# Kernel optimization log

Measured on AMD Instinct MI355X. Metric: run time of the kernel, lower is better.

The kernel has to match this reference:

```python
import jax, jax.numpy as jnp
import numpy as np
import itertools

N_SET = 4        # number of elements in the input set (input.size(-2))
IN_F = 2048      # in_features
OUT_F = 2048     # out_features
BOT = 512        # bottleneck_dim
B = 512          # batch size
NUM_NODES = 391
EMB_DIM = 300

# All nonempty subsets of range(N_SET), ordered by scale then lexicographic,
# exactly matching the torch loop over scales / itertools.combinations.
SUBSETS = [c for s in range(1, N_SET + 1) for c in itertools.combinations(range(N_SET), s)]

def _incl_matrix():
    # M[i, j] = 1 if SUBSETS[j] is a subset of SUBSETS[i].
    # This reproduces the dict-based scatter-sum: the aggregated output for rset
    # is the sum of raw Relation outputs over all nonempty k \subseteq rset.
    masks = [sum(1 << i for i in c) for c in SUBSETS]
    n = len(masks)
    M = np.zeros((n, n), dtype=np.float32)
    for i, mi in enumerate(masks):
        for j, mj in enumerate(masks):
            if (mj & mi) == mj:
                M[i, j] = 1.0
    return M

INCL = _incl_matrix()  # [15, 15]

def setup_inputs():
    key = jax.random.key(0)
    ks = jax.random.split(key, 16)
    inp = {"x": jax.random.normal(ks[0], (B, N_SET, IN_F), dtype=jnp.float32)}
    ki = 1
    for s in range(1, N_SET + 1):
        fan = s * IN_F
        inp[f"w1_s{s}"] = jax.random.normal(ks[ki], (BOT, fan), dtype=jnp.float32) / np.float32(np.sqrt(fan)); ki += 1
        inp[f"b1_s{s}"] = jnp.zeros((BOT,), dtype=jnp.float32)
        inp[f"w2_s{s}"] = jax.random.normal(ks[ki], (OUT_F, BOT), dtype=jnp.float32) / np.float32(np.sqrt(BOT)); ki += 1
        inp[f"b2_s{s}"] = jnp.zeros((OUT_F,), dtype=jnp.float32)
    inp["w_emb"] = jax.random.normal(ks[ki], (EMB_DIM, OUT_F), dtype=jnp.float32) / np.float32(np.sqrt(OUT_F)); ki += 1
    inp["b_emb"] = jnp.zeros((EMB_DIM,), dtype=jnp.float32)
    inp["w_node"] = jax.random.normal(ks[ki], (NUM_NODES, OUT_F), dtype=jnp.float32) / np.float32(np.sqrt(OUT_F)); ki += 1
    inp["b_node"] = jnp.zeros((NUM_NODES,), dtype=jnp.float32)
    return inp

def _base_forward(x, ws):
    # Batched per-scale Relation MLPs over all C(4,s) subsets at once.
    raws = []
    for s in range(1, N_SET + 1):
        idx = np.array(list(itertools.combinations(range(N_SET), s)))  # [C, s]
        g = x[:, idx, :]                                  # [B, C, s, F] gather
        h = g.reshape(g.shape[0], g.shape[1], s * IN_F)   # concat along subset
        w1, b1, w2, b2 = ws[s - 1]
        h = jax.nn.relu(h)
        h = jax.nn.relu(jnp.einsum('bcf,of->bco', h, w1) + b1)
        raws.append(jnp.einsum('bcd,od->bco', h, w2) + b2)  # [B, C, OUT_F]
    raw = jnp.concatenate(raws, axis=1)  # [B, 15, OUT_F]
    # Subset-inclusion scatter-sum, expressed as a dense 15x15 contraction.
    return jnp.einsum('ij,bjf->bif', jnp.asarray(INCL), raw)

def reference(x, w1_s1, b1_s1, w2_s1, b2_s1, w1_s2, b1_s2, w2_s2, b2_s2,
              w1_s3, b1_s3, w2_s3, b2_s3, w1_s4, b1_s4, w2_s4, b2_s4,
              w_emb, b_emb, w_node, b_node):
    ws = [(w1_s1, b1_s1, w2_s1, b2_s1), (w1_s2, b1_s2, w2_s2, b2_s2),
          (w1_s3, b1_s3, w2_s3, b2_s3), (w1_s4, b1_s4, w2_s4, b2_s4)]
    feats = _base_forward(x, ws)                              # [B, 15, OUT_F]
    embeddings = jnp.einsum('bnf,ef->bne', feats, w_emb) + b_emb  # [B, 15, 300]
    node_out = jnp.einsum('bnf,vf->bnv', feats, w_node) + b_node  # [B, 15, 391]
    return embeddings, jnp.swapaxes(node_out, -2, -1)             # [B, 391, 15]
```

## Files before the change

kernel.cpp:

```cpp
#include <hip/hip_runtime.h>
#include <stdint.h>

using bf16x8 = __attribute__((ext_vector_type(8))) short;
using f32x4  = __attribute__((ext_vector_type(4))) float;

#define DEVINL __device__ __forceinline__

DEVINL unsigned short f2bf(float f) {
  union { float f; unsigned u; } v; v.f = f;
  unsigned u = v.u;
  return (unsigned short)((u + 0x7FFFu + ((u >> 16) & 1u)) >> 16);
}
DEVINL float bf2f(unsigned short h) {
  union { unsigned u; float f; } v; v.u = ((unsigned)h) << 16;
  return v.f;
}

DEVINL void gload_lds16(const void* g, void* l) {
  __builtin_amdgcn_global_load_lds(
      (const __attribute__((address_space(1))) void*)g,
      (__attribute__((address_space(3))) void*)l, 16, 0, 0);
}

template<int OUT_BF16, int HAS_BIAS>
DEVINL void gemm_core(const unsigned short* __restrict__ A,
                      const unsigned short* __restrict__ B,
                      void* __restrict__ C,
                      const float* __restrict__ bias,
                      int K, int Cld, int arow0, int brow0, int crow0, int ccol0)
{
  __shared__ __align__(16) unsigned short As[3][256 * 64];
  __shared__ __align__(16) unsigned short Bs[3][128 * 64];

  const int t    = threadIdx.x;
  const int wave = t >> 6;
  const int lane = t & 63;
  const int wr   = (wave >> 1) << 6;
  const int wc   = (wave & 1) << 6;
  const int lrow = lane & 15;
  const int kg   = lane >> 4;

  f32x4 acc[4][4];
#pragma unroll
  for (int r = 0; r < 4; ++r)
#pragma unroll
    for (int q = 0; q < 4; ++q) acc[r][q] = (f32x4){0.f, 0.f, 0.f, 0.f};

  const int srow = t >> 3;
  const int scol = (((t & 7) ^ (srow & 7)) << 3);
  const unsigned short* aSrc = A + (size_t)(arow0 + srow) * K + scol;
  const unsigned short* bSrc = B + (size_t)(brow0 + srow) * K + scol;

  auto STAGE_S0 = [&](int slot, int kt) {
    const int k0 = kt << 6;
    char* aD = (char*)As[slot] + wave * 1024;
    char* bD = (char*)Bs[slot] + wave * 1024;
    gload_lds16(aSrc + (size_t)0 * K + k0, aD);
    gload_lds16(aSrc + (size_t)64 * K + k0, aD + 8192);
    gload_lds16(bSrc + (size_t)0 * K + k0, bD);
  };
  auto STAGE_S1 = [&](int slot, int kt) {
    const int k0 = kt << 6;
    char* aD = (char*)As[slot] + wave * 1024;
    char* bD = (char*)Bs[slot] + wave * 1024;
    gload_lds16(aSrc + (size_t)128 * K + k0, aD + 16384);
    gload_lds16(aSrc + (size_t)192 * K + k0, aD + 24576);
    gload_lds16(bSrc + (size_t)64 * K + k0, bD + 8192);
  };

  const int nt = K >> 6;
  STAGE_S0(0, 0); STAGE_S1(0, 0);
  if (nt > 1) { STAGE_S0(1, 1); STAGE_S1(1, 1); }

  const int rs = lrow & 7;
  const int cA0 = ((kg + 0) ^ rs) << 3;
  const int cA1 = ((kg + 4) ^ rs) << 3;

  if (nt > 1) { asm volatile("s_waitcnt vmcnt(6)" ::: "memory"); }
  else        { asm volatile("s_waitcnt vmcnt(0)" ::: "memory"); }
  __builtin_amdgcn_s_barrier();

  int sl = 0;
  for (int kt = 0; kt < nt; ++kt) {
    const unsigned short* Ab = As[sl];
    const unsigned short* Bb = Bs[sl];
    int s2 = sl + 2; if (s2 >= 3) s2 -= 3;

    bf16x8 af[4], bq[4];
#pragma unroll
    for (int r = 0; r < 4; ++r)
      af[r] = *(const bf16x8*)&Ab[(wr + r * 16 + lrow) * 64 + cA0];
#pragma unroll
    for (int q = 0; q < 4; ++q)
      bq[q] = *(const bf16x8*)&Bb[(wc + q * 16 + lrow) * 64 + cA0];
    if (kt + 2 < nt) STAGE_S0(s2, kt + 2);
    __builtin_amdgcn_s_barrier();
    __builtin_amdgcn_s_setprio(1);
#pragma unroll
    for (int r = 0; r < 4; ++r)
#pragma unroll
      for (int q = 0; q < 4; ++q)
        acc[r][q] = __builtin_amdgcn_mfma_f32_16x16x32_bf16(af[r], bq[q], acc[r][q], 0, 0, 0);
    __builtin_amdgcn_s_setprio(0);
    __builtin_amdgcn_s_barrier();

#pragma unroll
    for (int r = 0; r < 4; ++r)
      af[r] = *(const bf16x8*)&Ab[(wr + r * 16 + lrow) * 64 + cA1];
#pragma unroll
    for (int q = 0; q < 4; ++q)
      bq[q] = *(const bf16x8*)&Bb[(wc + q * 16 + lrow) * 64 + cA1];
    if (kt + 2 < nt) {
      STAGE_S1(s2, kt + 2);
      asm volatile("s_waitcnt vmcnt(6)" ::: "memory");
    } else if (kt + 1 < nt) {
      asm volatile("s_waitcnt vmcnt(0)" ::: "memory");
    }
    __builtin_amdgcn_s_barrier();
    __builtin_amdgcn_s_setprio(1);
#pragma unroll
    for (int r = 0; r < 4; ++r)
#pragma unroll
      for (int q = 0; q < 4; ++q)
        acc[r][q] = __builtin_amdgcn_mfma_f32_16x16x32_bf16(af[r], bq[q], acc[r][q], 0, 0, 0);
    __builtin_amdgcn_s_setprio(0);
    __builtin_amdgcn_s_barrier();

    ++sl; if (sl == 3) sl = 0;
  }

#pragma unroll
  for (int r = 0; r < 4; ++r) {
#pragma unroll
    for (int q = 0; q < 4; ++q) {
      const int col = ccol0 + wc + q * 16 + lrow;
      const float bv = HAS_BIAS ? bias[col] : 0.f;
#pragma unroll
      for (int v = 0; v < 4; ++v) {
        const int row = crow0 + wr + r * 16 + (kg << 2) + v;
        const float val = acc[r][q][v] + bv;
        if (OUT_BF16)
          ((unsigned short*)C)[(size_t)row * Cld + col] = f2bf(val);
        else
          ((float*)C)[(size_t)row * Cld + col] = val;
      }
    }
  }
}

__global__ __launch_bounds__(512) void mega1_k(const unsigned short* __restrict__ xrb,
                                               const unsigned short* __restrict__ w1cat,
                                               const unsigned short* __restrict__ wen,
                                               const unsigned short* __restrict__ w2t,
                                               unsigned short* __restrict__ H0p,
                                               unsigned short* __restrict__ W2EN) {
  const int bid = blockIdx.x;
  if (bid < 160) {
    const int p = bid >> 3, q = bid & 7;
    const int rt = q >> 2, ct = q & 3;
    const int MM[20] = {0,1,2,3, 0,1,2, 1,2,3, 0,1, 1,2, 2,3, 0,1,2,3};
    const int JJ[20] = {0,0,0,0, 1,1,1, 2,2,2, 3,3, 4,4, 5,5, 6,7,8,9};
    gemm_core<1, 0>(xrb, w1cat, H0p, nullptr, 2048, 512,
                    MM[p] * 512 + rt * 256, JJ[p] * 512 + ct * 128,
                    p * 512 + rt * 256, ct * 128);
  } else {
    const int b2 = bid - 160;
    const int s = b2 / 12, r = b2 % 12;
    const int rt = r >> 2, ct = r & 3;
    gemm_core<1, 0>(wen, w2t, W2EN, nullptr, 2048, 512,
                    rt * 256, s * 512 + ct * 128,
                    s * 768 + rt * 256, ct * 128);
  }
}

__global__ __launch_bounds__(512) void gemmF_k(const unsigned short* __restrict__ h1,
                                               const unsigned short* __restrict__ W2EN,
                                               const float* __restrict__ ENb,
                                               float* __restrict__ EN0) {
  const int y = blockIdx.y;
  const int c = y >> 1;
  const int s = (c < 4) ? 1 : (c < 10) ? 2 : (c < 14) ? 3 : 4;
  gemm_core<0, 1>(h1, W2EN, EN0, ENb + (size_t)(s - 1) * 768, 512, 768,
                  y * 256, (s - 1) * 768 + blockIdx.x * 128,
                  y * 256, blockIdx.x * 128);
}

__global__ __launch_bounds__(256) void prep_all_k(const float* __restrict__ x,
                                                  const float* w11, const float* w12,
                                                  const float* w13, const float* w14,
                                                  const float* w21, const float* w22,
                                                  const float* w23, const float* w24,
                                                  const float* __restrict__ wemb,
                                                  const float* __restrict__ wnode,
                                                  const float* b21, const float* b22,
                                                  const float* b23, const float* b24,
                                                  unsigned short* __restrict__ xrb,
                                                  unsigned short* __restrict__ w1cat,
                                                  unsigned short* __restrict__ w2t,
                                                  unsigned short* __restrict__ wen,
                                                  float* __restrict__ ENb) {
  __shared__ float lds[64][65];
  __shared__ float red[4][4];
  const int bid = blockIdx.x;
  if (bid < 10240) {
    const int tid = bid * 256 + threadIdx.x;
    const int r = tid >> 9;
    const int k = (tid & 511) << 2;
    const int j = r >> 9, o = r & 511;
    const float* src; int s, tt;
    if (j == 0)      { src = w11; s = 1; tt = 0; }
    else if (j < 3)  { src = w12; s = 2; tt = j - 1; }
    else if (j < 6)  { src = w13; s = 3; tt = j - 3; }
    else             { src = w14; s = 4; tt = j - 6; }
    const float4 vv = *(const float4*)(src + (size_t)o * (s * 2048) + tt * 2048 + k);
    ushort4 ov;
    ov.x = f2bf(vv.x); ov.y = f2bf(vv.y); ov.z = f2bf(vv.z); ov.w = f2bf(vv.w);
    *(ushort4*)(w1cat + (size_t)r * 2048 + k) = ov;
  } else if (bid < 14336) {
    const int tid = (bid - 10240) * 256 + threadIdx.x;
    const int r = tid >> 9;
    const int k = (tid & 511) << 2;
    const int m = r >> 9, b = r & 511;
    const float4 vv = *(const float4*)(x + ((size_t)(b * 4 + m)) * 2048 + k);
    ushort4 o;
    o.x = f2bf(fmaxf(vv.x, 0.f)); o.y = f2bf(fmaxf(vv.y, 0.f));
    o.z = f2bf(fmaxf(vv.z, 0.f)); o.w = f2bf(fmaxf(vv.w, 0.f));
    *(ushort4*)(xrb + (size_t)r * 2048 + k) = o;
  } else if (bid < 15360) {
    const int idx = bid - 14336;
    const int s = idx >> 8, rem = idx & 255;
    const int rt = rem >> 3, ct = rem & 7;
    const float* src = (s == 0) ? w21 : (s == 1) ? w22 : (s == 2) ? w23 : w24;
    const int tr = threadIdx.x >> 4;
    const int tc = (threadIdx.x & 15) << 2;
#pragma unroll
    for (int i = 0; i < 4; ++i) {
      const float4 v = *(const float4*)(src + (size_t)(rt * 64 + tr + 16 * i) * 512 + ct * 64 + tc);
      lds[tr + 16 * i][tc + 0] = v.x; lds[tr + 16 * i][tc + 1] = v.y;
      lds[tr + 16 * i][tc + 2] = v.z; lds[tr + 16 * i][tc + 3] = v.w;
    }
    __syncthreads();
#pragma unroll
    for (int i = 0; i < 4; ++i) {
      ushort4 ov;
      ov.x = f2bf(lds[tc + 0][tr + 16 * i]); ov.y = f2bf(lds[tc + 1][tr + 16 * i]);
      ov.z = f2bf(lds[tc + 2][tr + 16 * i]); ov.w = f2bf(lds[tc + 3][tr + 16 * i]);
      *(ushort4*)(w2t + ((size_t)s * 512 + ct * 64 + tr + 16 * i) * 2048 + rt * 64 + tc) = ov;
    }
  } else if (bid < 16896) {
    const int tid = (bid - 15360) * 256 + threadIdx.x;
    const int r = tid >> 9;
    const int k = (tid & 511) << 2;
    float4 vv = make_float4(0.f, 0.f, 0.f, 0.f);
    if (r < 300)       vv = *(const float4*)(wemb + (size_t)r * 2048 + k);
    else if (r < 691)  vv = *(const float4*)(wnode + (size_t)(r - 300) * 2048 + k);
    ushort4 ov;
    ov.x = f2bf(vv.x); ov.y = f2bf(vv.y); ov.z = f2bf(vv.z); ov.w = f2bf(vv.w);
    *(ushort4*)(wen + (size_t)r * 2048 + k) = ov;
  } else {
    const int e = bid - 16896;
    const int t8 = threadIdx.x << 3;
    float a0 = 0.f, a1 = 0.f, a2 = 0.f, a3 = 0.f;
    if (e < 691) {
      const float* row = (e < 300) ? (wemb + (size_t)e * 2048)
                                   : (wnode + (size_t)(e - 300) * 2048);
      const float4 r0 = *(const float4*)(row + t8);
      const float4 r1 = *(const float4*)(row + t8 + 4);
      const float4 c10 = *(const float4*)(b21 + t8), c11 = *(const float4*)(b21 + t8 + 4);
      const float4 c20 = *(const float4*)(b22 + t8), c21 = *(const float4*)(b22 + t8 + 4);
      const float4 c30 = *(const float4*)(b23 + t8), c31 = *(const float4*)(b23 + t8 + 4);
      const float4 c40 = *(const float4*)(b24 + t8), c41 = *(const float4*)(b24 + t8 + 4);
      a0 = r0.x*c10.x + r0.y*c10.y + r0.z*c10.z + r0.w*c10.w
         + r1.x*c11.x + r1.y*c11.y + r1.z*c11.z + r1.w*c11.w;
      a1 = r0.x*c20.x + r0.y*c20.y + r0.z*c20.z + r0.w*c20.w
         + r1.x*c21.x + r1.y*c21.y + r1.z*c21.z + r1.w*c21.w;
      a2 = r0.x*c30.x + r0.y*c30.y + r0.z*c30.z + r0.w*c30.w
         + r1.x*c31.x + r1.y*c31.y + r1.z*c31.z + r1.w*c31.w;
      a3 = r0.x*c40.x + r0.y*c40.y + r0.z*c40.z + r0.w*c40.w
         + r1.x*c41.x + r1.y*c41.y + r1.z*c41.z + r1.w*c41.w;
    }
#pragma unroll
    for (int off = 32; off; off >>= 1) {
      a0 += __shfl_down(a0, off); a1 += __shfl_down(a1, off);
      a2 += __shfl_down(a2, off); a3 += __shfl_down(a3, off);
    }
    const int wv = threadIdx.x >> 6;
    if ((threadIdx.x & 63) == 0) {
      red[wv][0] = a0; red[wv][1] = a1; red[wv][2] = a2; red[wv][3] = a3;
    }
    __syncthreads();
    if (threadIdx.x < 4) {
      const float v = red[0][threadIdx.x] + red[1][threadIdx.x] +
                      red[2][threadIdx.x] + red[3][threadIdx.x];
      ENb[(size_t)threadIdx.x * 768 + e] = (e < 691) ? v : 0.f;
    }
  }
}

__global__ __launch_bounds__(128) void combine1_k(const unsigned short* __restrict__ H0p,
                                                  unsigned short* __restrict__ h1,
                                                  const float* __restrict__ b11,
                                                  const float* __restrict__ b12,
                                                  const float* __restrict__ b13,
                                                  const float* __restrict__ b14) {
  const int cb = blockIdx.x;
  const int c = cb >> 9, b = cb & 511;
  const int s = (c < 4) ? 1 : (c < 10) ? 2 : (c < 14) ? 3 : 4;
  const unsigned char P[15][4] = {
    {0,0,0,0},{1,0,0,0},{2,0,0,0},{3,0,0,0},
    {4,7,0,0},{4,8,0,0},{4,9,0,0},{5,8,0,0},{5,9,0,0},{6,9,0,0},
    {10,12,14,0},{10,12,15,0},{10,13,15,0},{11,13,15,0},
    {16,17,18,19}};
  const float* b1 = (s == 1) ? b11 : (s == 2) ? b12 : (s == 3) ? b13 : b14;
  const int o = threadIdx.x << 2;
  float4 a = *(const float4*)(b1 + o);
  for (int t = 0; t < s; ++t) {
    const int p = P[c][t];
    const ushort4 hv = *(const ushort4*)(H0p + ((size_t)(p * 512 + b)) * 512 + o);
    a.x += bf2f(hv.x); a.y += bf2f(hv.y); a.z += bf2f(hv.z); a.w += bf2f(hv.w);
  }
  ushort4 ov;
  ov.x = f2bf(fmaxf(a.x, 0.f)); ov.y = f2bf(fmaxf(a.y, 0.f));
  ov.z = f2bf(fmaxf(a.z, 0.f)); ov.w = f2bf(fmaxf(a.w, 0.f));
  *(ushort4*)(h1 + (size_t)cb * 512 + o) = ov;
}

__global__ __launch_bounds__(256) void combine2_k(const float* __restrict__ EN0,
                                                  const float* __restrict__ b_emb,
                                                  const float* __restrict__ b_node,
                                                  float* __restrict__ out0,
                                                  float* __restrict__ out1) {
  const int b   = blockIdx.x;
  const int col = blockIdx.y * 256 + threadIdx.x;
  if (col >= 691) return;
  float vals[15];
#pragma unroll
  for (int j = 0; j < 15; ++j)
    vals[j] = EN0[((size_t)(j * 512 + b)) * 768 + col];
  const int MSK[15] = {1,2,4,8,3,5,9,6,10,12,7,11,13,14,15};
  if (col < 300) {
    const float be = b_emb[col];
#pragma unroll
    for (int i = 0; i < 15; ++i) {
      float sum = be;
#pragma unroll
      for (int j = 0; j < 15; ++j)
        if ((MSK[j] & MSK[i]) == MSK[j]) sum += vals[j];
      out0[((size_t)b * 15 + i) * 300 + col] = sum;
    }
  } else {
    const int v = col - 300;
    const float bn = b_node[v];
#pragma unroll
    for (int i = 0; i < 15; ++i) {
      float sum = bn;
#pragma unroll
      for (int j = 0; j < 15; ++j)
        if ((MSK[j] & MSK[i]) == MSK[j]) sum += vals[j];
      out1[((size_t)b * 391 + v) * 15 + i] = sum;
    }
  }
}

extern "C" void kernel_launch(void* const* d_in, const int* in_sizes, int n_in,
                              void* d_out, int out_size, void* d_ws, size_t ws_size,
                              hipStream_t stream) {
  const float* x     = (const float*)d_in[0];
  const float* w11   = (const float*)d_in[1];
  const float* b11   = (const float*)d_in[2];
  const float* w21   = (const float*)d_in[3];
  const float* b21   = (const float*)d_in[4];
  const float* w12   = (const float*)d_in[5];
  const float* b12   = (const float*)d_in[6];
  const float* w22   = (const float*)d_in[7];
  const float* b22   = (const float*)d_in[8];
  const float* w13   = (const float*)d_in[9];
  const float* b13   = (const float*)d_in[10];
  const float* w23   = (const float*)d_in[11];
  const float* b23   = (const float*)d_in[12];
  const float* w14   = (const float*)d_in[13];
  const float* b14   = (const float*)d_in[14];
  const float* w24   = (const float*)d_in[15];
  const float* b24   = (const float*)d_in[16];
  const float* wemb  = (const float*)d_in[17];
  const float* bemb  = (const float*)d_in[18];
  const float* wnode = (const float*)d_in[19];
  const float* bnode = (const float*)d_in[20];

  char* ws = (char*)d_ws;
  unsigned short* xrb   = (unsigned short*)(ws + 0);
  unsigned short* w1cat = (unsigned short*)(ws + 8388608);
  unsigned short* w2t   = (unsigned short*)(ws + 29360128);
  unsigned short* wen   = (unsigned short*)(ws + 37748736);
  unsigned short* H0p   = (unsigned short*)(ws + 40894464);
  unsigned short* W2EN  = (unsigned short*)(ws + 51380224);
  float*          ENb   = (float*)(ws + 54525952);
  unsigned short* h1bf  = (unsigned short*)(ws + 54538240);
  float*          EN0   = (float*)(ws + 0);

  float* out0 = (float*)d_out;
  float* out1 = out0 + 2304000;

  prep_all_k<<<17664, 256, 0, stream>>>(x, w11, w12, w13, w14, w21, w22, w23, w24,
                                        wemb, wnode, b21, b22, b23, b24,
                                        xrb, w1cat, w2t, wen, ENb);
  mega1_k   <<<208, 512, 0, stream>>>(xrb, w1cat, wen, w2t, H0p, W2EN);
  combine1_k<<<7680, 128, 0, stream>>>(H0p, h1bf, b11, b12, b13, b14);
  gemmF_k   <<<dim3(6, 30), 512, 0, stream>>>(h1bf, W2EN, ENb, EN0);
  combine2_k<<<dim3(512, 3), 256, 0, stream>>>(EN0, bemb, bnode, out0, out1);
}
```

Measured before the change: 92.46 us.

## Use 256x256 split-K tiles in first GEMM stage and reduce halves in combine

The first mega kernel switches from 256x128 tiles over full K to 256x256 tiles over half of K, writing two bf16 partial outputs per GEMM. The combine1 kernel gains extra blocks that sum the two partial halves for H0 and W2EN. The aim is more MFMA work per staged byte and the same block count with larger tiles, at the cost of extra partial-sum memory traffic and an extra bf16 rounding step. A double-buffered pipeline with interleaved staging and priority hints replaces the triple-buffered core for this stage.

```diff
diff --git a/kernel.cpp b/kernel.cpp
--- a/kernel.cpp
+++ b/kernel.cpp
@@ -20,6 +20,140 @@
   __builtin_amdgcn_global_load_lds(
       (const __attribute__((address_space(1))) void*)g,
       (__attribute__((address_space(3))) void*)l, 16, 0, 0);
+}
+
+DEVINL void gemm_core256(const unsigned short* __restrict__ A,
+                         const unsigned short* __restrict__ B,
+                         unsigned short* __restrict__ C,
+                         int Klen, int ld, int Cld,
+                         int arow0, int brow0, int crow0, int ccol0, int kofs)
+{
+  __shared__ __align__(16) unsigned short As[2][256 * 64];
+  __shared__ __align__(16) unsigned short Bs[2][256 * 64];
+
+  const int t    = threadIdx.x;
+  const int wave = t >> 6;
+  const int lane = t & 63;
+  const int wr   = (wave >> 2) << 7;
+  const int wc   = (wave & 3) << 6;
+  const int lrow = lane & 15;
+  const int kg   = lane >> 4;
+
+  f32x4 acc[8][4];
+#pragma unroll
+  for (int r = 0; r < 8; ++r)
+#pragma unroll
+    for (int q = 0; q < 4; ++q) acc[r][q] = (f32x4){0.f, 0.f, 0.f, 0.f};
+
+  const int srow = t >> 3;
+  const int scol = (((t & 7) ^ (srow & 7)) << 3);
+  const unsigned short* aSrc = A + (size_t)(arow0 + srow) * ld + kofs + scol;
+  const unsigned short* bSrc = B + (size_t)(brow0 + srow) * ld + kofs + scol;
+
+  auto STAGE_A = [&](int buf, int kt) {
+    const int k0 = kt << 6;
+    char* aD = (char*)As[buf] + wave * 1024;
+#pragma unroll
+    for (int p = 0; p < 4; ++p)
+      gload_lds16(aSrc + (size_t)(p * 64) * ld + k0, aD + p * 8192);
+  };
+  auto STAGE_B = [&](int buf, int kt) {
+    const int k0 = kt << 6;
+    char* bD = (char*)Bs[buf] + wave * 1024;
+#pragma unroll
+    for (int p = 0; p < 4; ++p)
+      gload_lds16(bSrc + (size_t)(p * 64) * ld + k0, bD + p * 8192);
+  };
+
+  const int nt = Klen >> 6;
+  STAGE_A(0, 0); STAGE_B(0, 0);
+  asm volatile("s_waitcnt vmcnt(0)" ::: "memory");
+  __builtin_amdgcn_s_barrier();
+
+  const int rs = lrow & 7;
+  const int cA0 = ((kg + 0) ^ rs) << 3;
+  const int cA1 = ((kg + 4) ^ rs) << 3;
+
+  bf16x8 a[4], b[4];
+  for (int kt = 0; kt < nt; ++kt) {
+    const unsigned short* Ab = As[kt & 1];
+    const unsigned short* Bb = Bs[kt & 1];
+    const int nbuf = (kt + 1) & 1;
+
+#pragma unroll
+    for (int r = 0; r < 4; ++r)
+      a[r] = *(const bf16x8*)&Ab[(wr + r * 16 + lrow) * 64 + cA0];
+#pragma unroll
+    for (int q = 0; q < 4; ++q)
+      b[q] = *(const bf16x8*)&Bb[(wc + q * 16 + lrow) * 64 + cA0];
+    if (kt + 1 < nt) STAGE_A(nbuf, kt + 1);
+    __builtin_amdgcn_s_barrier();
+    __builtin_amdgcn_s_setprio(1);
+#pragma unroll
+    for (int r = 0; r < 4; ++r)
+#pragma unroll
+      for (int q = 0; q < 4; ++q)
+        acc[r][q] = __builtin_amdgcn_mfma_f32_16x16x32_bf16(a[r], b[q], acc[r][q], 0, 0, 0);
+    __builtin_amdgcn_s_setprio(0);
+    __builtin_amdgcn_s_barrier();
+
+#pragma unroll
+    for (int r = 0; r < 4; ++r)
+      a[r] = *(const bf16x8*)&Ab[(wr + 64 + r * 16 + lrow) * 64 + cA0];
+    if (kt + 1 < nt) STAGE_B(nbuf, kt + 1);
+    __builtin_amdgcn_s_barrier();
+    __builtin_amdgcn_s_setprio(1);
+#pragma unroll
+    for (int r = 0; r < 4; ++r)
+#pragma unroll
+      for (int q = 0; q < 4; ++q)
+        acc[4 + r][q] = __builtin_amdgcn_mfma_f32_16x16x32_bf16(a[r], b[q], acc[4 + r][q], 0, 0, 0);
+    __builtin_amdgcn_s_setprio(0);
+    __builtin_amdgcn_s_barrier();
+
+#pragma unroll
+    for (int r = 0; r < 4; ++r)
+      a[r] = *(const bf16x8*)&Ab[(wr + r * 16 + lrow) * 64 + cA1];
+#pragma unroll
+    for (int q = 0; q < 4; ++q)
+      b[q] = *(const bf16x8*)&Bb[(wc + q * 16 + lrow) * 64 + cA1];
+    __builtin_amdgcn_s_barrier();
+    __builtin_amdgcn_s_setprio(1);
+#pragma unroll
+    for (int r = 0; r < 4; ++r)
+#pragma unroll
+      for (int q = 0; q < 4; ++q)
+        acc[r][q] = __builtin_amdgcn_mfma_f32_16x16x32_bf16(a[r], b[q], acc[r][q], 0, 0, 0);
+    __builtin_amdgcn_s_setprio(0);
+    __builtin_amdgcn_s_barrier();
+
+#pragma unroll
+    for (int r = 0; r < 4; ++r)
+      a[r] = *(const bf16x8*)&Ab[(wr + 64 + r * 16 + lrow) * 64 + cA1];
+    if (kt + 1 < nt)
+      asm volatile("s_waitcnt vmcnt(0)" ::: "memory");
+    __builtin_amdgcn_s_barrier();
+    __builtin_amdgcn_s_setprio(1);
+#pragma unroll
+    for (int r = 0; r < 4; ++r)
+#pragma unroll
+      for (int q = 0; q < 4; ++q)
+        acc[4 + r][q] = __builtin_amdgcn_mfma_f32_16x16x32_bf16(a[r], b[q], acc[4 + r][q], 0, 0, 0);
+    __builtin_amdgcn_s_setprio(0);
+    __builtin_amdgcn_s_barrier();
+  }
+
+#pragma unroll
+  for (int rr = 0; rr < 8; ++rr) {
+#pragma unroll
+    for (int q = 0; q < 4; ++q) {
+      const int col = ccol0 + wc + q * 16 + lrow;
+      const int rowb = crow0 + wr + (rr >> 2) * 64 + (rr & 3) * 16 + (kg << 2);
+#pragma unroll
+      for (int v = 0; v < 4; ++v)
+        C[(size_t)(rowb + v) * Cld + col] = f2bf(acc[rr][q][v]);
+    }
+  }
 }
 
 template<int OUT_BF16, int HAS_BIAS>
@@ -152,24 +286,25 @@
                                                const unsigned short* __restrict__ w1cat,
                                                const unsigned short* __restrict__ wen,
                                                const unsigned short* __restrict__ w2t,
-                                               unsigned short* __restrict__ H0p,
-                                               unsigned short* __restrict__ W2EN) {
+                                               unsigned short* __restrict__ H0h,
+                                               unsigned short* __restrict__ W2ENh) {
   const int bid = blockIdx.x;
   if (bid < 160) {
-    const int p = bid >> 3, q = bid & 7;
-    const int rt = q >> 2, ct = q & 3;
+    const int p = bid >> 3, rem = bid & 7;
+    const int kh = rem & 1, rt = (rem >> 1) & 1, ct = rem >> 2;
     const int MM[20] = {0,1,2,3, 0,1,2, 1,2,3, 0,1, 1,2, 2,3, 0,1,2,3};
     const int JJ[20] = {0,0,0,0, 1,1,1, 2,2,2, 3,3, 4,4, 5,5, 6,7,8,9};
-    gemm_core<1, 0>(xrb, w1cat, H0p, nullptr, 2048, 512,
-                    MM[p] * 512 + rt * 256, JJ[p] * 512 + ct * 128,
-                    p * 512 + rt * 256, ct * 128);
+    gemm_core256(xrb, w1cat, H0h + (size_t)kh * 5242880, 1024, 2048, 512,
+                 MM[p] * 512 + rt * 256, JJ[p] * 512 + ct * 256,
+                 p * 512 + rt * 256, ct * 256, kh * 1024);
   } else {
     const int b2 = bid - 160;
     const int s = b2 / 12, r = b2 % 12;
-    const int rt = r >> 2, ct = r & 3;
-    gemm_core<1, 0>(wen, w2t, W2EN, nullptr, 2048, 512,
-                    rt * 256, s * 512 + ct * 128,
-                    s * 768 + rt * 256, ct * 128);
+    const int kh = r & 1, tt = r >> 1;
+    const int rt = tt >> 1, ct = tt & 1;
+    gemm_core256(wen, w2t, W2ENh + (size_t)kh * 1572864, 1024, 2048, 512,
+                 rt * 256, s * 512 + ct * 256,
+                 s * 768 + rt * 256, ct * 256, kh * 1024);
   }
 }
 
@@ -297,32 +432,50 @@
   }
 }
 
-__global__ __launch_bounds__(128) void combine1_k(const unsigned short* __restrict__ H0p,
+__global__ __launch_bounds__(128) void combine1_k(const unsigned short* __restrict__ H0h,
                                                   unsigned short* __restrict__ h1,
                                                   const float* __restrict__ b11,
                                                   const float* __restrict__ b12,
                                                   const float* __restrict__ b13,
-                                                  const float* __restrict__ b14) {
-  const int cb = blockIdx.x;
-  const int c = cb >> 9, b = cb & 511;
-  const int s = (c < 4) ? 1 : (c < 10) ? 2 : (c < 14) ? 3 : 4;
-  const unsigned char P[15][4] = {
-    {0,0,0,0},{1,0,0,0},{2,0,0,0},{3,0,0,0},
-    {4,7,0,0},{4,8,0,0},{4,9,0,0},{5,8,0,0},{5,9,0,0},{6,9,0,0},
-    {10,12,14,0},{10,12,15,0},{10,13,15,0},{11,13,15,0},
-    {16,17,18,19}};
-  const float* b1 = (s == 1) ? b11 : (s == 2) ? b12 : (s == 3) ? b13 : b14;
-  const int o = threadIdx.x << 2;
-  float4 a = *(const float4*)(b1 + o);
-  for (int t = 0; t < s; ++t) {
-    const int p = P[c][t];
-    const ushort4 hv = *(const ushort4*)(H0p + ((size_t)(p * 512 + b)) * 512 + o);
-    a.x += bf2f(hv.x); a.y += bf2f(hv.y); a.z += bf2f(hv.z); a.w += bf2f(hv.w);
-  }
-  ushort4 ov;
-  ov.x = f2bf(fmaxf(a.x, 0.f)); ov.y = f2bf(fmaxf(a.y, 0.f));
-  ov.z = f2bf(fmaxf(a.z, 0.f)); ov.w = f2bf(fmaxf(a.w, 0.f));
-  *(ushort4*)(h1 + (size_t)cb * 512 + o) = ov;
+                                                  const float* __restrict__ b14,
+                                                  const unsigned short* __restrict__ W2ENh,
+                                                  unsigned short* __restrict__ W2EN) {
+  const int bid = blockIdx.x;
+  if (bid < 7680) {
+    const int cb = bid;
+    const int c = cb >> 9, b = cb & 511;
+    const int s = (c < 4) ? 1 : (c < 10) ? 2 : (c < 14) ? 3 : 4;
+    const unsigned char P[15][4] = {
+      {0,0,0,0},{1,0,0,0},{2,0,0,0},{3,0,0,0},
+      {4,7,0,0},{4,8,0,0},{4,9,0,0},{5,8,0,0},{5,9,0,0},{6,9,0,0},
+      {10,12,14,0},{10,12,15,0},{10,13,15,0},{11,13,15,0},
+      {16,17,18,19}};
+    const float* b1 = (s == 1) ? b11 : (s == 2) ? b12 : (s == 3) ? b13 : b14;
+    const int o = threadIdx.x << 2;
+    float4 a = *(const float4*)(b1 + o);
+    for (int t = 0; t < s; ++t) {
+      const int p = P[c][t];
+      const size_t base = ((size_t)(p * 512 + b)) * 512 + o;
+      const ushort4 h0 = *(const ushort4*)(H0h + base);
+      const ushort4 h1v = *(const ushort4*)(H0h + 5242880 + base);
+      a.x += bf2f(h0.x) + bf2f(h1v.x); a.y += bf2f(h0.y) + bf2f(h1v.y);
+      a.z += bf2f(h0.z) + bf2f(h1v.z); a.w += bf2f(h0.w) + bf2f(h1v.w);
+    }
+    ushort4 ov;
+    ov.x = f2bf(fmaxf(a.x, 0.f)); ov.y = f2bf(fmaxf(a.y, 0.f));
+    ov.z = f2bf(fmaxf(a.z, 0.f)); ov.w = f2bf(fmaxf(a.w, 0.f));
+    *(ushort4*)(h1 + (size_t)cb * 512 + o) = ov;
+  } else {
+    const int idx = bid - 7680;
+    const size_t off = (size_t)idx * 1024 + (size_t)threadIdx.x * 8;
+    const bf16x8 a0 = *(const bf16x8*)(W2ENh + off);
+    const bf16x8 a1 = *(const bf16x8*)(W2ENh + 1572864 + off);
+    bf16x8 ov;
+#pragma unroll
+    for (int i = 0; i < 8; ++i)
+      ov[i] = (short)f2bf(bf2f((unsigned short)a0[i]) + bf2f((unsigned short)a1[i]));
+    *(bf16x8*)(W2EN + off) = ov;
+  }
 }
 
 __global__ __launch_bounds__(256) void combine2_k(const float* __restrict__ EN0,
@@ -392,10 +545,11 @@
   unsigned short* w1cat = (unsigned short*)(ws + 8388608);
   unsigned short* w2t   = (unsigned short*)(ws + 29360128);
   unsigned short* wen   = (unsigned short*)(ws + 37748736);
-  unsigned short* H0p   = (unsigned short*)(ws + 40894464);
-  unsigned short* W2EN  = (unsigned short*)(ws + 51380224);
-  float*          ENb   = (float*)(ws + 54525952);
-  unsigned short* h1bf  = (unsigned short*)(ws + 54538240);
+  unsigned short* H0h   = (unsigned short*)(ws + 40894464);
+  unsigned short* W2ENh = (unsigned short*)(ws + 61865984);
+  unsigned short* W2EN  = (unsigned short*)(ws + 68157440);
+  float*          ENb   = (float*)(ws + 71303168);
+  unsigned short* h1bf  = (unsigned short*)(ws + 71315456);
   float*          EN0   = (float*)(ws + 0);
 
   float* out0 = (float*)d_out;
@@ -404,8 +558,8 @@
   prep_all_k<<<17664, 256, 0, stream>>>(x, w11, w12, w13, w14, w21, w22, w23, w24,
                                         wemb, wnode, b21, b22, b23, b24,
                                         xrb, w1cat, w2t, wen, ENb);
-  mega1_k   <<<208, 512, 0, stream>>>(xrb, w1cat, wen, w2t, H0p, W2EN);
-  combine1_k<<<7680, 128, 0, stream>>>(H0p, h1bf, b11, b12, b13, b14);
+  mega1_k   <<<208, 512, 0, stream>>>(xrb, w1cat, wen, w2t, H0h, W2ENh);
+  combine1_k<<<9216, 128, 0, stream>>>(H0h, h1bf, b11, b12, b13, b14, W2ENh, W2EN);
   gemmF_k   <<<dim3(6, 30), 512, 0, stream>>>(h1bf, W2EN, ENb, EN0);
   combine2_k<<<dim3(512, 3), 256, 0, stream>>>(EN0, bemb, bnode, out0, out1);
 }
```

New measurement: 95.79 us. 3.6% more time.
